# Performance work log

Measured on AMD Instinct MI355X. Metric: run time of the kernel, lower is better.

The kernel has to match this reference:

```python
import jax, jax.numpy as jnp
import numpy as np

B, T, HID = 2, 2048, 1024
H, HKV, D = 16, 4, 64          # query heads, kv heads, head dim
GLR = 16                        # gate low-rank dim
GATE_LOGIT_NORMALIZER = 16.0
EPS = 1e-6


def setup_inputs() -> dict:
    key = jax.random.key(0)
    ks = jax.random.split(key, 8)
    w = lambda k, shape: jax.random.normal(k, shape, jnp.float32) * 0.02
    return dict(
        hidden_states=jax.random.normal(ks[0], (B, T, HID), jnp.float32),
        Wq=w(ks[1], (HID, H * D)),
        Wk=w(ks[2], (HID, HKV * D)),
        Wv=w(ks[3], (HID, HKV * D)),
        Wo=w(ks[4], (H * D, HID)),
        Wg1=w(ks[5], (HID, GLR)),
        Wg2=w(ks[6], (GLR, HKV * D)),
        bg2=jnp.zeros((HKV * D,), jnp.float32),
        g_norm_weight=jnp.ones((D,), jnp.float32),
    )


def _gla(q, k, v, g):
    """Gated linear attention recurrence.
    q,k,v,g: [B,H,T,D]. State S: [B,H,D,Dv].
    S_t = exp(g_t)[:,None]*S_{t-1} + k_t (outer) v_t ; o_t = (q_t*scale) @ S_t.
    Equivalent math to chunk_gla / fused_recurrent_gla (default scale=D**-0.5).
    """
    scale = q.shape[-1] ** -0.5
    qs = jnp.moveaxis(q * scale, 2, 0)   # [T,B,H,D]
    ks_ = jnp.moveaxis(k, 2, 0)
    vs = jnp.moveaxis(v, 2, 0)
    gs = jnp.moveaxis(g, 2, 0)
    S0 = jnp.zeros(q.shape[:2] + (q.shape[-1], v.shape[-1]), q.dtype)

    def step(S, inp):
        qt, kt, vt, gt = inp
        S = jnp.exp(gt)[..., None] * S + kt[..., None] * vt[..., None, :]
        o = jnp.einsum('bhk,bhkv->bhv', qt, S)
        return S, o

    S, o = jax.lax.scan(step, S0, (qs, ks_, vs, gs))
    return jnp.moveaxis(o, 0, 2), S      # [B,H,T,Dv]


def reference(hidden_states, Wq, Wk, Wv, Wo, Wg1, Wg2, bg2, g_norm_weight):
    b, t, _ = hidden_states.shape
    split = lambda x, h: jnp.transpose(x.reshape(b, t, h, D), (0, 2, 1, 3))  # [B,h,T,D]
    # projections + relu feature map on q,k
    q = jax.nn.relu(split(hidden_states @ Wq, H))
    k = jax.nn.relu(split(hidden_states @ Wk, HKV))
    v = split(hidden_states @ Wv, HKV)
    # low-rank gate -> logsigmoid / normalizer (log-space decay)
    gk = jax.nn.log_sigmoid(split((hidden_states @ Wg1) @ Wg2 + bg2, HKV)) / GATE_LOGIT_NORMALIZER
    # GQA expansion (repeat_interleave over head dim)
    rep = lambda x: jnp.repeat(x, H // HKV, axis=1)
    o, _ = _gla(q, rep(k), rep(v), rep(gk))        # [B,H,T,D]
    o = jnp.transpose(o, (0, 2, 1, 3))              # [B,T,H,D]
    # per-head RMSNorm over head_dim
    var = jnp.mean(jnp.square(o), axis=-1, keepdims=True)
    o = g_norm_weight * (o * jax.lax.rsqrt(var + EPS))
    return o.reshape(b, t, H * D) @ Wo
```

## Files before the change

kernel.cpp:

```cpp
#include <hip/hip_runtime.h>
#include <hip/hip_bf16.h>
#include <math.h>

#define B_    2
#define T_    2048
#define HID_  1024
#define H_    16
#define HKV_  4
#define D_    64
#define GLR_  16
#define NTOK  (B_*T_)
#define KVD   (HKV_*D_)
#define KVSTR 512
#define QD    (H_*D_)
#define NPROJ (QD+KVSTR)
#define CHUNK 64
#define NC    (T_/CHUNK)
#define SCALE 0.125f
#define EPS_  1e-6f

typedef __attribute__((ext_vector_type(8))) short short8;
typedef __attribute__((ext_vector_type(4))) float f32x4;

__device__ __forceinline__ ushort f2b(float f) {
  __hip_bfloat16 h = __float2bfloat16(f);
  return *reinterpret_cast<ushort*>(&h);
}
__device__ __forceinline__ float b2f(ushort u) {
  __hip_bfloat16 h = *reinterpret_cast<__hip_bfloat16*>(&u);
  return __bfloat162float(h);
}

__device__ __forceinline__ void gload16(const ushort* g, ushort* l) {
  __builtin_amdgcn_global_load_lds(
      (const __attribute__((address_space(1))) unsigned int*)g,
      (__attribute__((address_space(3))) unsigned int*)l, 16, 0, 0);
}

__global__ __launch_bounds__(256) void stage_all(const float* __restrict__ h,
                                                 const float* __restrict__ Wq,
                                                 const float* __restrict__ Wk,
                                                 const float* __restrict__ Wv,
                                                 const float* __restrict__ Wo,
                                                 const float* __restrict__ Wg1,
                                                 ushort* __restrict__ hb,
                                                 ushort* __restrict__ Wqt,
                                                 ushort* __restrict__ Wkvt,
                                                 ushort* __restrict__ Wot,
                                                 ushort* __restrict__ Wg1t) {
  __shared__ ushort tile[64][65];
  int bi = blockIdx.x;
  if (bi < 4096) {
    int i = bi * 256 + threadIdx.x;
    float4 v = *(const float4*)(h + (size_t)i * 4);
    ushort4 o; o.x = f2b(v.x); o.y = f2b(v.y); o.z = f2b(v.z); o.w = f2b(v.w);
    *(ushort4*)(hb + (size_t)i * 4) = o;
    return;
  }
  bi -= 4096;
  if (bi < 64) {
    int idx = bi * 256 + threadIdx.x;
    int kk = idx >> 4, n = idx & 15;
    Wg1t[(size_t)n * HID_ + kk] = f2b(Wg1[(size_t)kk * GLR_ + n]);
    return;
  }
  bi -= 64;
  const float* W; ushort* Wt; int K, N, nb_, kb_;
  if (bi < 256)      { W = Wq; Wt = Wqt;  K = HID_; N = QD;  nb_ = bi & 15; kb_ = bi >> 4; }
  else if (bi < 320) { bi -= 256; W = Wk; Wt = Wkvt; K = HID_; N = KVD; nb_ = bi & 3; kb_ = bi >> 2; }
  else if (bi < 384) { bi -= 320; W = Wv; Wt = Wkvt + (size_t)KVD * HID_; K = HID_; N = KVD; nb_ = bi & 3; kb_ = bi >> 2; }
  else               { bi -= 384; W = Wo; Wt = Wot;  K = QD;  N = HID_; nb_ = bi & 15; kb_ = bi >> 4; }
  int n0 = nb_ * 64, k0 = kb_ * 64;
  for (int idx = threadIdx.x; idx < 64 * 64; idx += 256) {
    int r = idx >> 6, c = idx & 63;
    tile[c][r] = f2b(W[(size_t)(k0 + r) * N + n0 + c]);
  }
  __syncthreads();
  for (int idx = threadIdx.x; idx < 64 * 64; idx += 256) {
    int r = idx >> 6, c = idx & 63;
    Wt[(size_t)(n0 + r) * K + k0 + c] = tile[r][c];
  }
}

__global__ __launch_bounds__(256) void gemm_proj(const ushort* __restrict__ A,
                                                 const ushort* __restrict__ Bt,
                                                 ushort* __restrict__ qb,
                                                 ushort* __restrict__ kvb) {
  __shared__ ushort As[128][32];
  __shared__ ushort Bs[128][32];
  const int t = threadIdx.x;
  const int rowBase = blockIdx.y * 128, colBase = blockIdx.x * 128;
  const int lane = t & 63, w = t >> 6;
  const int wr = w >> 1, wc = w & 1;
  const int lrow = lane & 15, hi = lane >> 4;
  const int K = HID_;
  f32x4 acc[4][4];
#pragma unroll
  for (int mi = 0; mi < 4; ++mi)
#pragma unroll
    for (int ni = 0; ni < 4; ++ni) acc[mi][ni] = (f32x4){0.f, 0.f, 0.f, 0.f};

  for (int k0 = 0; k0 < K; k0 += 32) {
#pragma unroll
    for (int l = 0; l < 2; ++l) {
      int idx = t + (l << 8);
      int row = idx >> 2, ch = (idx & 3) << 3;
      gload16(&A [(size_t)(rowBase + row) * K + k0 + ch], &As[0][0] + idx * 8);
      gload16(&Bt[(size_t)(colBase + row) * K + k0 + ch], &Bs[0][0] + idx * 8);
    }
    __syncthreads();
    short8 af[4], bf[4];
#pragma unroll
    for (int mi = 0; mi < 4; ++mi)
      af[mi] = *(const short8*)&As[wr * 64 + mi * 16 + lrow][hi * 8];
#pragma unroll
    for (int ni = 0; ni < 4; ++ni)
      bf[ni] = *(const short8*)&Bs[wc * 64 + ni * 16 + lrow][hi * 8];
#pragma unroll
    for (int mi = 0; mi < 4; ++mi)
#pragma unroll
      for (int ni = 0; ni < 4; ++ni)
        acc[mi][ni] = __builtin_amdgcn_mfma_f32_16x16x32_bf16(af[mi], bf[ni], acc[mi][ni], 0, 0, 0);
    __syncthreads();
  }
#pragma unroll
  for (int mi = 0; mi < 4; ++mi)
#pragma unroll
    for (int ni = 0; ni < 4; ++ni)
#pragma unroll
      for (int r = 0; r < 4; ++r) {
        int gm = rowBase + wr * 64 + mi * 16 + hi * 4 + r;
        int gn = colBase + wc * 64 + ni * 16 + lrow;
        float val = acc[mi][ni][r];
        if (gn < QD) qb[(size_t)gm * QD + gn] = f2b(fmaxf(val, 0.f));
        else         kvb[(size_t)gm * KVSTR + gn - QD] = f2b(val);
      }
}

__global__ __launch_bounds__(256) void gemm_bf16_mfma(const ushort* __restrict__ A,
                                                      const ushort* __restrict__ Bt,
                                                      float* __restrict__ C,
                                                      int M, int N, int K) {
  __shared__ ushort As[128][32];
  __shared__ ushort Bs[128][32];
  const int t = threadIdx.x;
  const int rowBase = blockIdx.y * 128, colBase = blockIdx.x * 128;
  const int lane = t & 63, w = t >> 6;
  const int wr = w >> 1, wc = w & 1;
  const int lrow = lane & 15, hi = lane >> 4;
  f32x4 acc[4][4];
#pragma unroll
  for (int mi = 0; mi < 4; ++mi)
#pragma unroll
    for (int ni = 0; ni < 4; ++ni) acc[mi][ni] = (f32x4){0.f, 0.f, 0.f, 0.f};

  for (int k0 = 0; k0 < K; k0 += 32) {
#pragma unroll
    for (int l = 0; l < 2; ++l) {
      int idx = t + (l << 8);
      int row = idx >> 2, ch = (idx & 3) << 3;
      gload16(&A [(size_t)(rowBase + row) * K + k0 + ch], &As[0][0] + idx * 8);
      gload16(&Bt[(size_t)(colBase + row) * K + k0 + ch], &Bs[0][0] + idx * 8);
    }
    __syncthreads();
    short8 af[4], bf[4];
#pragma unroll
    for (int mi = 0; mi < 4; ++mi)
      af[mi] = *(const short8*)&As[wr * 64 + mi * 16 + lrow][hi * 8];
#pragma unroll
    for (int ni = 0; ni < 4; ++ni)
      bf[ni] = *(const short8*)&Bs[wc * 64 + ni * 16 + lrow][hi * 8];
#pragma unroll
    for (int mi = 0; mi < 4; ++mi)
#pragma unroll
      for (int ni = 0; ni < 4; ++ni)
        acc[mi][ni] = __builtin_amdgcn_mfma_f32_16x16x32_bf16(af[mi], bf[ni], acc[mi][ni], 0, 0, 0);
    __syncthreads();
  }
#pragma unroll
  for (int mi = 0; mi < 4; ++mi)
#pragma unroll
    for (int ni = 0; ni < 4; ++ni)
#pragma unroll
      for (int r = 0; r < 4; ++r) {
        int gm = rowBase + wr * 64 + mi * 16 + hi * 4 + r;
        int gn = colBase + wc * 64 + ni * 16 + lrow;
        C[(size_t)gm * N + gn] = acc[mi][ni][r];
      }
}

__global__ __launch_bounds__(256) void gate_cumsum(const ushort* __restrict__ hb,
                                                   const ushort* __restrict__ Wg1t,
                                                   const float* __restrict__ Wg2,
                                                   const float* __restrict__ bg2,
                                                   float* __restrict__ bc) {
  __shared__ float gts[CHUNK][GLR_ + 1];
  const int t = threadIdx.x, lane = t & 63, w = t >> 6;
  const int lrow = lane & 15, hi = lane >> 4;
  const int c0 = blockIdx.x * CHUNK;
  const int b = c0 / T_, tloc = c0 % T_;
  {
    f32x4 acc = (f32x4){0.f, 0.f, 0.f, 0.f};
#pragma unroll
    for (int kk = 0; kk < 32; ++kk) {
      int k0 = kk * 32 + hi * 8;
      short8 a = *(const short8*)&hb[(size_t)(c0 + w * 16 + lrow) * HID_ + k0];
      short8 bf = *(const short8*)&Wg1t[(size_t)lrow * HID_ + k0];
      acc = __builtin_amdgcn_mfma_f32_16x16x32_bf16(a, bf, acc, 0, 0, 0);
    }
#pragma unroll
    for (int r = 0; r < 4; ++r) gts[w * 16 + hi * 4 + r][lrow] = acc[r];
  }
  __syncthreads();
  {
    const int c = t;
    const int j = c >> 6, d = c & 63;
    const int gj = b * HKV_ + j;
    const float bias = bg2[c];
    float run = 0.f;
    size_t base = ((size_t)gj * T_ + tloc) * D_ + d;
    for (int tok = 0; tok < CHUNK; ++tok) {
      float acc2 = bias;
#pragma unroll
      for (int r = 0; r < GLR_; ++r) acc2 += gts[tok][r] * Wg2[r * KVD + c];
      float ls = fminf(acc2, 0.f) - log1pf(expf(-fabsf(acc2)));
      run += ls * (1.0f / 16.0f);
      bc[base + (size_t)tok * D_] = run;
    }
  }
}

__global__ __launch_bounds__(256) void chunk_kv(const ushort* __restrict__ kvb,
                                                const float* __restrict__ bc,
                                                float* __restrict__ Mt,
                                                float* __restrict__ E) {
  __shared__ ushort vts[64][72];
  __shared__ ushort kts[64][72];
  __shared__ float blast[D_];
  int blk = blockIdx.x;
  int c = blk % NC, gj = blk / NC;
  int b = gj >> 2, j = gj & 3;
  size_t kb = ((size_t)(b * T_ + c * CHUNK)) * KVSTR + j * D_;
  size_t bb = ((size_t)gj * T_ + c * CHUNK) * D_;
  const int t = threadIdx.x, lane = t & 63, w = t >> 6;
  const int lrow = lane & 15, hi = lane >> 4;
  if (t < D_) blast[t] = bc[bb + (size_t)(CHUNK - 1) * D_ + t];
  __syncthreads();
  for (int idx = t; idx < CHUNK * D_; idx += 256) {
    int tt = idx >> 6, col = idx & 63;
    float bv = bc[bb + idx];
    kts[col][tt] = f2b(fmaxf(b2f(kvb[kb + (size_t)tt * KVSTR + col]), 0.f) * expf(blast[col] - bv));
    vts[col][tt] = kvb[kb + (size_t)tt * KVSTR + 256 + col];
  }
  __syncthreads();
#pragma unroll
  for (int ni = 0; ni < 4; ++ni) {
    f32x4 acc = (f32x4){0.f, 0.f, 0.f, 0.f};
#pragma unroll
    for (int kk = 0; kk < 2; ++kk) {
      short8 a  = *(const short8*)&vts[w * 16 + lrow][kk * 32 + hi * 8];
      short8 bf = *(const short8*)&kts[ni * 16 + lrow][kk * 32 + hi * 8];
      acc = __builtin_amdgcn_mfma_f32_16x16x32_bf16(a, bf, acc, 0, 0, 0);
    }
#pragma unroll
    for (int r = 0; r < 4; ++r)
      Mt[(size_t)blk * D_ * D_ + (size_t)(w * 16 + hi * 4 + r) * D_ + ni * 16 + lrow] = acc[r];
  }
  if (t < D_) E[(size_t)blk * D_ + t] = expf(blast[t]);
}

__global__ __launch_bounds__(256) void state_scan(const float* __restrict__ Mt,
                                                  const float* __restrict__ E,
                                                  float* __restrict__ Sbt) {
  int gj = blockIdx.x >> 4;
  int elem = ((blockIdx.x & 15) << 8) + threadIdx.x;
  int i = elem & 63;
  float S = 0.f;
#pragma unroll
  for (int c = 0; c < NC; ++c) {
    size_t base = ((size_t)gj * NC + c) * (D_ * D_) + elem;
    Sbt[base] = S;
    S = E[((size_t)gj * NC + c) * D_ + i] * S + Mt[base];
  }
}

__global__ __launch_bounds__(256) void gla_out(const ushort* __restrict__ qb,
                                               const ushort* __restrict__ kvb,
                                               const float* __restrict__ bc,
                                               const float* __restrict__ Sbt,
                                               const float* __restrict__ gw,
                                               ushort* __restrict__ obh) {
  __shared__ ushort qes[64][72];
  __shared__ ushort kes[64][72];
  __shared__ ushort vts[64][72];
  __shared__ ushort sts[64][72];
  __shared__ ushort Al [64][72];
  int blk = blockIdx.x;
  int c = blk % NC, bh = blk / NC;
  int b = bh / H_, h = bh % H_;
  int j = h >> 2, gj = b * HKV_ + j;
  size_t nb = (size_t)(b * T_ + c * CHUNK);
  size_t bb = ((size_t)gj * T_ + c * CHUNK) * D_;
  size_t sbase = ((size_t)gj * NC + c) * D_ * D_;
  const int t = threadIdx.x, lane = t & 63, w = t >> 6;
  const int lrow = lane & 15, hi = lane >> 4;
  for (int idx = t; idx < CHUNK * D_; idx += 256) {
    int tt = idx >> 6, col = idx & 63;
    float bv = bc[bb + idx];
    qes[tt][col] = f2b(b2f(qb[(nb + tt) * QD + h * D_ + col]) * expf(bv) * SCALE);
    kes[tt][col] = f2b(fmaxf(b2f(kvb[(nb + tt) * KVSTR + j * D_ + col]), 0.f) * expf(-bv));
    vts[col][tt] = kvb[(nb + tt) * KVSTR + 256 + j * D_ + col];
    sts[tt][col] = f2b(Sbt[sbase + idx]);
  }
  __syncthreads();
  {
    const int ti = w;
#pragma unroll
    for (int si = 0; si < 4; ++si) {
      f32x4 acc = (f32x4){0.f, 0.f, 0.f, 0.f};
      if (si <= ti) {
#pragma unroll
        for (int kk = 0; kk < 2; ++kk) {
          short8 a  = *(const short8*)&qes[ti * 16 + lrow][kk * 32 + hi * 8];
          short8 bf = *(const short8*)&kes[si * 16 + lrow][kk * 32 + hi * 8];
          acc = __builtin_amdgcn_mfma_f32_16x16x32_bf16(a, bf, acc, 0, 0, 0);
        }
      }
#pragma unroll
      for (int r = 0; r < 4; ++r) {
        int grow = ti * 16 + hi * 4 + r, gcol = si * 16 + lrow;
        Al[grow][gcol] = f2b(gcol <= grow ? acc[r] : 0.f);
      }
    }
  }
  __syncthreads();
  {
    float o[4][4];
#pragma unroll
    for (int ni = 0; ni < 4; ++ni) {
      f32x4 acc = (f32x4){0.f, 0.f, 0.f, 0.f};
#pragma unroll
      for (int kk = 0; kk < 2; ++kk) {
        short8 a  = *(const short8*)&qes[w * 16 + lrow][kk * 32 + hi * 8];
        short8 bf = *(const short8*)&sts[ni * 16 + lrow][kk * 32 + hi * 8];
        acc = __builtin_amdgcn_mfma_f32_16x16x32_bf16(a, bf, acc, 0, 0, 0);
      }
#pragma unroll
      for (int kk = 0; kk < 2; ++kk) {
        short8 a  = *(const short8*)&Al[w * 16 + lrow][kk * 32 + hi * 8];
        short8 bf = *(const short8*)&vts[ni * 16 + lrow][kk * 32 + hi * 8];
        acc = __builtin_amdgcn_mfma_f32_16x16x32_bf16(a, bf, acc, 0, 0, 0);
      }
#pragma unroll
      for (int r = 0; r < 4; ++r) o[ni][r] = acc[r];
    }
#pragma unroll
    for (int r = 0; r < 4; ++r) {
      float ss = o[0][r] * o[0][r] + o[1][r] * o[1][r]
               + o[2][r] * o[2][r] + o[3][r] * o[3][r];
      ss += __shfl_xor(ss, 1, 64);
      ss += __shfl_xor(ss, 2, 64);
      ss += __shfl_xor(ss, 4, 64);
      ss += __shfl_xor(ss, 8, 64);
      float inv = rsqrtf(ss * (1.0f / D_) + EPS_);
      size_t rowoff = (nb + w * 16 + hi * 4 + r) * QD + h * D_;
#pragma unroll
      for (int ni = 0; ni < 4; ++ni) {
        int d = ni * 16 + lrow;
        obh[rowoff + d] = f2b(gw[d] * o[ni][r] * inv);
      }
    }
  }
}

extern "C" void kernel_launch(void* const* d_in, const int* in_sizes, int n_in,
                              void* d_out, int out_size, void* d_ws, size_t ws_size,
                              hipStream_t stream) {
  const float* h   = (const float*)d_in[0];
  const float* Wq  = (const float*)d_in[1];
  const float* Wk  = (const float*)d_in[2];
  const float* Wv  = (const float*)d_in[3];
  const float* Wo  = (const float*)d_in[4];
  const float* Wg1 = (const float*)d_in[5];
  const float* Wg2 = (const float*)d_in[6];
  const float* bg2 = (const float*)d_in[7];
  const float* gw  = (const float*)d_in[8];
  float* out = (float*)d_out;

  ushort* qb   = (ushort*)d_ws;
  ushort* kvb  = qb   + (size_t)NTOK * QD;
  ushort* hb   = kvb  + (size_t)NTOK * KVSTR;
  ushort* Wqt  = hb   + (size_t)NTOK * HID_;
  ushort* Wkvt = Wqt  + (size_t)HID_ * QD;
  ushort* Wot  = Wkvt + (size_t)KVSTR * HID_;
  ushort* Wg1t = Wot  + (size_t)HID_ * QD;
  float* bc  = (float*)(Wg1t + (size_t)GLR_ * HID_);
  float* Sbt = bc + (size_t)B_ * HKV_ * T_ * D_;
  float* Mt  = Sbt + (size_t)B_ * HKV_ * NC * D_ * D_;
  float* E   = Mt + (size_t)B_ * HKV_ * NC * D_ * D_;
  ushort* obh = hb;

  dim3 blk(256);
  stage_all<<<4800, blk, 0, stream>>>(h, Wq, Wk, Wv, Wo, Wg1, hb, Wqt, Wkvt, Wot, Wg1t);
  gemm_proj<<<dim3(NPROJ / 128, NTOK / 128), blk, 0, stream>>>(hb, Wqt, qb, kvb);
  gate_cumsum<<<NTOK / CHUNK, blk, 0, stream>>>(hb, Wg1t, Wg2, bg2, bc);
  chunk_kv<<<B_ * HKV_ * NC, blk, 0, stream>>>(kvb, bc, Mt, E);
  state_scan<<<B_ * HKV_ * 16, blk, 0, stream>>>(Mt, E, Sbt);
  gla_out<<<B_ * H_ * NC, blk, 0, stream>>>(qb, kvb, bc, Sbt, gw, obh);
  gemm_bf16_mfma<<<dim3(HID_ / 128, NTOK / 128), blk, 0, stream>>>(obh, Wot, out, NTOK, HID_, HID_);
}
```

Baseline: 200.8 us.

## Merge projection GEMM with gate kernel, halve GEMM M-tiles, store chunk states as bf16

```diff
diff --git a/kernel.cpp b/kernel.cpp
--- a/kernel.cpp
+++ b/kernel.cpp
@@ -18,6 +18,7 @@
 #define NC    (T_/CHUNK)
 #define SCALE 0.125f
 #define EPS_  1e-6f
+#define NPROJBLK ((NPROJ/128)*(NTOK/64))
 
 typedef __attribute__((ext_vector_type(8))) short short8;
 typedef __attribute__((ext_vector_type(4))) float f32x4;
@@ -82,129 +83,76 @@
   }
 }
 
-__global__ __launch_bounds__(256) void gemm_proj(const ushort* __restrict__ A,
+__global__ __launch_bounds__(256) void proj_gate(const ushort* __restrict__ A,
                                                  const ushort* __restrict__ Bt,
+                                                 const ushort* __restrict__ Wg1t,
+                                                 const float* __restrict__ Wg2,
+                                                 const float* __restrict__ bg2,
                                                  ushort* __restrict__ qb,
-                                                 ushort* __restrict__ kvb) {
-  __shared__ ushort As[128][32];
+                                                 ushort* __restrict__ kvb,
+                                                 float* __restrict__ bc) {
+  __shared__ ushort As[64][32];
   __shared__ ushort Bs[128][32];
-  const int t = threadIdx.x;
-  const int rowBase = blockIdx.y * 128, colBase = blockIdx.x * 128;
-  const int lane = t & 63, w = t >> 6;
-  const int wr = w >> 1, wc = w & 1;
-  const int lrow = lane & 15, hi = lane >> 4;
-  const int K = HID_;
-  f32x4 acc[4][4];
-#pragma unroll
-  for (int mi = 0; mi < 4; ++mi)
-#pragma unroll
-    for (int ni = 0; ni < 4; ++ni) acc[mi][ni] = (f32x4){0.f, 0.f, 0.f, 0.f};
-
-  for (int k0 = 0; k0 < K; k0 += 32) {
-#pragma unroll
-    for (int l = 0; l < 2; ++l) {
-      int idx = t + (l << 8);
-      int row = idx >> 2, ch = (idx & 3) << 3;
-      gload16(&A [(size_t)(rowBase + row) * K + k0 + ch], &As[0][0] + idx * 8);
-      gload16(&Bt[(size_t)(colBase + row) * K + k0 + ch], &Bs[0][0] + idx * 8);
-    }
-    __syncthreads();
-    short8 af[4], bf[4];
-#pragma unroll
-    for (int mi = 0; mi < 4; ++mi)
-      af[mi] = *(const short8*)&As[wr * 64 + mi * 16 + lrow][hi * 8];
-#pragma unroll
-    for (int ni = 0; ni < 4; ++ni)
-      bf[ni] = *(const short8*)&Bs[wc * 64 + ni * 16 + lrow][hi * 8];
-#pragma unroll
-    for (int mi = 0; mi < 4; ++mi)
-#pragma unroll
-      for (int ni = 0; ni < 4; ++ni)
-        acc[mi][ni] = __builtin_amdgcn_mfma_f32_16x16x32_bf16(af[mi], bf[ni], acc[mi][ni], 0, 0, 0);
-    __syncthreads();
-  }
-#pragma unroll
-  for (int mi = 0; mi < 4; ++mi)
-#pragma unroll
-    for (int ni = 0; ni < 4; ++ni)
-#pragma unroll
-      for (int r = 0; r < 4; ++r) {
-        int gm = rowBase + wr * 64 + mi * 16 + hi * 4 + r;
-        int gn = colBase + wc * 64 + ni * 16 + lrow;
-        float val = acc[mi][ni][r];
-        if (gn < QD) qb[(size_t)gm * QD + gn] = f2b(fmaxf(val, 0.f));
-        else         kvb[(size_t)gm * KVSTR + gn - QD] = f2b(val);
-      }
-}
-
-__global__ __launch_bounds__(256) void gemm_bf16_mfma(const ushort* __restrict__ A,
-                                                      const ushort* __restrict__ Bt,
-                                                      float* __restrict__ C,
-                                                      int M, int N, int K) {
-  __shared__ ushort As[128][32];
-  __shared__ ushort Bs[128][32];
-  const int t = threadIdx.x;
-  const int rowBase = blockIdx.y * 128, colBase = blockIdx.x * 128;
-  const int lane = t & 63, w = t >> 6;
-  const int wr = w >> 1, wc = w & 1;
-  const int lrow = lane & 15, hi = lane >> 4;
-  f32x4 acc[4][4];
-#pragma unroll
-  for (int mi = 0; mi < 4; ++mi)
-#pragma unroll
-    for (int ni = 0; ni < 4; ++ni) acc[mi][ni] = (f32x4){0.f, 0.f, 0.f, 0.f};
-
-  for (int k0 = 0; k0 < K; k0 += 32) {
-#pragma unroll
-    for (int l = 0; l < 2; ++l) {
-      int idx = t + (l << 8);
-      int row = idx >> 2, ch = (idx & 3) << 3;
-      gload16(&A [(size_t)(rowBase + row) * K + k0 + ch], &As[0][0] + idx * 8);
-      gload16(&Bt[(size_t)(colBase + row) * K + k0 + ch], &Bs[0][0] + idx * 8);
-    }
-    __syncthreads();
-    short8 af[4], bf[4];
-#pragma unroll
-    for (int mi = 0; mi < 4; ++mi)
-      af[mi] = *(const short8*)&As[wr * 64 + mi * 16 + lrow][hi * 8];
-#pragma unroll
-    for (int ni = 0; ni < 4; ++ni)
-      bf[ni] = *(const short8*)&Bs[wc * 64 + ni * 16 + lrow][hi * 8];
-#pragma unroll
-    for (int mi = 0; mi < 4; ++mi)
-#pragma unroll
-      for (int ni = 0; ni < 4; ++ni)
-        acc[mi][ni] = __builtin_amdgcn_mfma_f32_16x16x32_bf16(af[mi], bf[ni], acc[mi][ni], 0, 0, 0);
-    __syncthreads();
-  }
-#pragma unroll
-  for (int mi = 0; mi < 4; ++mi)
-#pragma unroll
-    for (int ni = 0; ni < 4; ++ni)
-#pragma unroll
-      for (int r = 0; r < 4; ++r) {
-        int gm = rowBase + wr * 64 + mi * 16 + hi * 4 + r;
-        int gn = colBase + wc * 64 + ni * 16 + lrow;
-        C[(size_t)gm * N + gn] = acc[mi][ni][r];
-      }
-}
-
-__global__ __launch_bounds__(256) void gate_cumsum(const ushort* __restrict__ hb,
-                                                   const ushort* __restrict__ Wg1t,
-                                                   const float* __restrict__ Wg2,
-                                                   const float* __restrict__ bg2,
-                                                   float* __restrict__ bc) {
   __shared__ float gts[CHUNK][GLR_ + 1];
   const int t = threadIdx.x, lane = t & 63, w = t >> 6;
   const int lrow = lane & 15, hi = lane >> 4;
-  const int c0 = blockIdx.x * CHUNK;
+  int bi = blockIdx.x;
+  if (bi < NPROJBLK) {
+    const int bx = bi % (NPROJ / 128), by = bi / (NPROJ / 128);
+    const int rowBase = by * 64, colBase = bx * 128;
+    const int wm = w >> 1, wn = w & 1;
+    f32x4 acc[2][4];
+#pragma unroll
+    for (int mi = 0; mi < 2; ++mi)
+#pragma unroll
+      for (int ni = 0; ni < 4; ++ni) acc[mi][ni] = (f32x4){0.f, 0.f, 0.f, 0.f};
+    for (int k0 = 0; k0 < HID_; k0 += 32) {
+      gload16(&A[(size_t)(rowBase + (t >> 2)) * HID_ + k0 + ((t & 3) << 3)],
+              &As[0][0] + t * 8);
+#pragma unroll
+      for (int l = 0; l < 2; ++l) {
+        int idx = t + (l << 8);
+        gload16(&Bt[(size_t)(colBase + (idx >> 2)) * HID_ + k0 + ((idx & 3) << 3)],
+                &Bs[0][0] + idx * 8);
+      }
+      __syncthreads();
+      short8 af[2], bf[4];
+#pragma unroll
+      for (int mi = 0; mi < 2; ++mi)
+        af[mi] = *(const short8*)&As[wm * 32 + mi * 16 + lrow][hi * 8];
+#pragma unroll
+      for (int ni = 0; ni < 4; ++ni)
+        bf[ni] = *(const short8*)&Bs[wn * 64 + ni * 16 + lrow][hi * 8];
+#pragma unroll
+      for (int mi = 0; mi < 2; ++mi)
+#pragma unroll
+        for (int ni = 0; ni < 4; ++ni)
+          acc[mi][ni] = __builtin_amdgcn_mfma_f32_16x16x32_bf16(af[mi], bf[ni], acc[mi][ni], 0, 0, 0);
+      __syncthreads();
+    }
+#pragma unroll
+    for (int mi = 0; mi < 2; ++mi)
+#pragma unroll
+      for (int ni = 0; ni < 4; ++ni)
+#pragma unroll
+        for (int r = 0; r < 4; ++r) {
+          int gm = rowBase + wm * 32 + mi * 16 + hi * 4 + r;
+          int gn = colBase + wn * 64 + ni * 16 + lrow;
+          float val = acc[mi][ni][r];
+          if (gn < QD) qb[(size_t)gm * QD + gn] = f2b(fmaxf(val, 0.f));
+          else         kvb[(size_t)gm * KVSTR + gn - QD] = f2b(val);
+        }
+    return;
+  }
+  bi -= NPROJBLK;
+  const int c0 = bi * CHUNK;
   const int b = c0 / T_, tloc = c0 % T_;
   {
     f32x4 acc = (f32x4){0.f, 0.f, 0.f, 0.f};
 #pragma unroll
     for (int kk = 0; kk < 32; ++kk) {
       int k0 = kk * 32 + hi * 8;
-      short8 a = *(const short8*)&hb[(size_t)(c0 + w * 16 + lrow) * HID_ + k0];
+      short8 a = *(const short8*)&A[(size_t)(c0 + w * 16 + lrow) * HID_ + k0];
       short8 bf = *(const short8*)&Wg1t[(size_t)lrow * HID_ + k0];
       acc = __builtin_amdgcn_mfma_f32_16x16x32_bf16(a, bf, acc, 0, 0, 0);
     }
@@ -228,6 +176,57 @@
       bc[base + (size_t)tok * D_] = run;
     }
   }
+}
+
+__global__ __launch_bounds__(256) void gemm_wo(const ushort* __restrict__ A,
+                                               const ushort* __restrict__ Bt,
+                                               float* __restrict__ C) {
+  __shared__ ushort As[64][32];
+  __shared__ ushort Bs[128][32];
+  const int t = threadIdx.x, lane = t & 63, w = t >> 6;
+  const int lrow = lane & 15, hi = lane >> 4;
+  const int rowBase = blockIdx.y * 64, colBase = blockIdx.x * 128;
+  const int wm = w >> 1, wn = w & 1;
+  const int N = HID_, K = HID_;
+  f32x4 acc[2][4];
+#pragma unroll
+  for (int mi = 0; mi < 2; ++mi)
+#pragma unroll
+    for (int ni = 0; ni < 4; ++ni) acc[mi][ni] = (f32x4){0.f, 0.f, 0.f, 0.f};
+  for (int k0 = 0; k0 < K; k0 += 32) {
+    gload16(&A[(size_t)(rowBase + (t >> 2)) * K + k0 + ((t & 3) << 3)],
+            &As[0][0] + t * 8);
+#pragma unroll
+    for (int l = 0; l < 2; ++l) {
+      int idx = t + (l << 8);
+      gload16(&Bt[(size_t)(colBase + (idx >> 2)) * K + k0 + ((idx & 3) << 3)],
+              &Bs[0][0] + idx * 8);
+    }
+    __syncthreads();
+    short8 af[2], bf[4];
+#pragma unroll
+    for (int mi = 0; mi < 2; ++mi)
+      af[mi] = *(const short8*)&As[wm * 32 + mi * 16 + lrow][hi * 8];
+#pragma unroll
+    for (int ni = 0; ni < 4; ++ni)
+      bf[ni] = *(const short8*)&Bs[wn * 64 + ni * 16 + lrow][hi * 8];
+#pragma unroll
+    for (int mi = 0; mi < 2; ++mi)
+#pragma unroll
+      for (int ni = 0; ni < 4; ++ni)
+        acc[mi][ni] = __builtin_amdgcn_mfma_f32_16x16x32_bf16(af[mi], bf[ni], acc[mi][ni], 0, 0, 0);
+    __syncthreads();
+  }
+#pragma unroll
+  for (int mi = 0; mi < 2; ++mi)
+#pragma unroll
+    for (int ni = 0; ni < 4; ++ni)
+#pragma unroll
+      for (int r = 0; r < 4; ++r) {
+        int gm = rowBase + wm * 32 + mi * 16 + hi * 4 + r;
+        int gn = colBase + wn * 64 + ni * 16 + lrow;
+        C[(size_t)gm * N + gn] = acc[mi][ni][r];
+      }
 }
 
 __global__ __launch_bounds__(256) void chunk_kv(const ushort* __restrict__ kvb,
@@ -271,7 +270,7 @@
 
 __global__ __launch_bounds__(256) void state_scan(const float* __restrict__ Mt,
                                                   const float* __restrict__ E,
-                                                  float* __restrict__ Sbt) {
+                                                  ushort* __restrict__ Sbtb) {
   int gj = blockIdx.x >> 4;
   int elem = ((blockIdx.x & 15) << 8) + threadIdx.x;
   int i = elem & 63;
@@ -279,7 +278,7 @@
 #pragma unroll
   for (int c = 0; c < NC; ++c) {
     size_t base = ((size_t)gj * NC + c) * (D_ * D_) + elem;
-    Sbt[base] = S;
+    Sbtb[base] = f2b(S);
     S = E[((size_t)gj * NC + c) * D_ + i] * S + Mt[base];
   }
 }
@@ -287,7 +286,7 @@
 __global__ __launch_bounds__(256) void gla_out(const ushort* __restrict__ qb,
                                                const ushort* __restrict__ kvb,
                                                const float* __restrict__ bc,
-                                               const float* __restrict__ Sbt,
+                                               const ushort* __restrict__ Sbtb,
                                                const float* __restrict__ gw,
                                                ushort* __restrict__ obh) {
   __shared__ ushort qes[64][72];
@@ -310,7 +309,7 @@
     qes[tt][col] = f2b(b2f(qb[(nb + tt) * QD + h * D_ + col]) * expf(bv) * SCALE);
     kes[tt][col] = f2b(fmaxf(b2f(kvb[(nb + tt) * KVSTR + j * D_ + col]), 0.f) * expf(-bv));
     vts[col][tt] = kvb[(nb + tt) * KVSTR + 256 + j * D_ + col];
-    sts[tt][col] = f2b(Sbt[sbase + idx]);
+    sts[tt][col] = Sbtb[sbase + idx];
   }
   __syncthreads();
   {
@@ -394,18 +393,17 @@
   ushort* Wkvt = Wqt  + (size_t)HID_ * QD;
   ushort* Wot  = Wkvt + (size_t)KVSTR * HID_;
   ushort* Wg1t = Wot  + (size_t)HID_ * QD;
-  float* bc  = (float*)(Wg1t + (size_t)GLR_ * HID_);
-  float* Sbt = bc + (size_t)B_ * HKV_ * T_ * D_;
-  float* Mt  = Sbt + (size_t)B_ * HKV_ * NC * D_ * D_;
+  ushort* Sbtb = Wg1t + (size_t)GLR_ * HID_;
+  float* bc  = (float*)(Sbtb + (size_t)B_ * HKV_ * NC * D_ * D_);
+  float* Mt  = bc + (size_t)B_ * HKV_ * T_ * D_;
   float* E   = Mt + (size_t)B_ * HKV_ * NC * D_ * D_;
   ushort* obh = hb;
 
   dim3 blk(256);
   stage_all<<<4800, blk, 0, stream>>>(h, Wq, Wk, Wv, Wo, Wg1, hb, Wqt, Wkvt, Wot, Wg1t);
-  gemm_proj<<<dim3(NPROJ / 128, NTOK / 128), blk, 0, stream>>>(hb, Wqt, qb, kvb);
-  gate_cumsum<<<NTOK / CHUNK, blk, 0, stream>>>(hb, Wg1t, Wg2, bg2, bc);
+  proj_gate<<<NPROJBLK + NTOK / CHUNK, blk, 0, stream>>>(hb, Wqt, Wg1t, Wg2, bg2, qb, kvb, bc);
   chunk_kv<<<B_ * HKV_ * NC, blk, 0, stream>>>(kvb, bc, Mt, E);
-  state_scan<<<B_ * HKV_ * 16, blk, 0, stream>>>(Mt, E, Sbt);
-  gla_out<<<B_ * H_ * NC, blk, 0, stream>>>(qb, kvb, bc, Sbt, gw, obh);
-  gemm_bf16_mfma<<<dim3(HID_ / 128, NTOK / 128), blk, 0, stream>>>(obh, Wot, out, NTOK, HID_, HID_);
-}
+  state_scan<<<B_ * HKV_ * 16, blk, 0, stream>>>(Mt, E, Sbtb);
+  gla_out<<<B_ * H_ * NC, blk, 0, stream>>>(qb, kvb, bc, Sbtb, gw, obh);
+  gemm_wo<<<dim3(HID_ / 128, NTOK / 64), blk, 0, stream>>>(obh, Wot, out);
+}
```

New measurement: 178.0 us. 1.13x faster.
